# Performance work log

Hardware: AMD Instinct MI355X
Metric: run time of the kernel (lower is better)

The kernel has to match this reference:

```python
import jax, jax.numpy as jnp
import numpy as np

N, IN_F, OUT_F = 4096, 512, 16
HID = [128, 64, 32]
H = 4  # num_head
LRELU_SLOPE = 0.2
BN_EPS = 1e-5
NEG_INF = -1e9


def _gat(x, adj_mask, W, a_src, a_dst, heads, f_out):
    n = x.shape[0]
    h = (x @ W).reshape(n, heads, f_out)              # [N,H,F]
    es = jnp.einsum('nhf,hf->hn', h, a_src)           # [H,N]
    ed = jnp.einsum('nhf,hf->hn', h, a_dst)           # [H,N]
    e = jax.nn.leaky_relu(es[:, :, None] + ed[:, None, :], LRELU_SLOPE)  # [H,N,N]
    e = jnp.where(adj_mask[None], e, NEG_INF)
    attn = jax.nn.softmax(e, axis=-1)                 # masked softmax over neighbors
    out = jnp.einsum('hij,jhf->ihf', attn, h)         # [N,H,F]
    return out.reshape(n, heads * f_out)


def _bn_elu(x, gamma, beta):
    mu = jnp.mean(x, axis=0)
    var = jnp.var(x, axis=0)
    xhat = (x - mu) * jax.lax.rsqrt(var + BN_EPS)
    return jax.nn.elu(xhat * gamma + beta)


def setup_inputs() -> dict:
    key = jax.random.key(0)
    ks = jax.random.split(key, 14)
    s = lambda fin: 1.0 / np.sqrt(fin)
    x = jax.random.normal(ks[0], (N, IN_F), jnp.float32)
    adj = jax.random.randint(ks[1], (N, N), 0, 2, jnp.int32)
    W1 = jax.random.normal(ks[2], (IN_F, H * HID[0]), jnp.float32) * s(IN_F)
    a1s = jax.random.normal(ks[3], (H, HID[0]), jnp.float32) * s(HID[0])
    a1d = jax.random.normal(ks[4], (H, HID[0]), jnp.float32) * s(HID[0])
    lw1 = jax.random.normal(ks[5], (H * HID[0], HID[1]), jnp.float32) * s(H * HID[0])
    lb1 = jnp.zeros((HID[1],), jnp.float32)
    g1 = jnp.ones((HID[1],), jnp.float32)
    be1 = jnp.zeros((HID[1],), jnp.float32)
    W2 = jax.random.normal(ks[6], (HID[1], H * HID[2]), jnp.float32) * s(HID[1])
    a2s = jax.random.normal(ks[7], (H, HID[2]), jnp.float32) * s(HID[2])
    a2d = jax.random.normal(ks[8], (H, HID[2]), jnp.float32) * s(HID[2])
    lw2 = jax.random.normal(ks[9], (H * HID[2], OUT_F), jnp.float32) * s(H * HID[2])
    lb2 = jnp.zeros((OUT_F,), jnp.float32)
    g2 = jnp.ones((OUT_F,), jnp.float32)
    be2 = jnp.zeros((OUT_F,), jnp.float32)
    return dict(x=x, adj=adj, W1=W1, a1s=a1s, a1d=a1d, lw1=lw1, lb1=lb1, g1=g1, be1=be1,
                W2=W2, a2s=a2s, a2d=a2d, lw2=lw2, lb2=lb2, g2=g2, be2=be2)


def reference(x, adj, W1, a1s, a1d, lw1, lb1, g1, be1, W2, a2s, a2d, lw2, lb2, g2, be2):
    adj_mask = adj > 0
    x1 = _gat(x, adj_mask, W1, a1s, a1d, H, HID[0])        # [N, H*128]
    x2 = _bn_elu(x1 @ lw1 + lb1, g1, be1)                  # [N, 64]
    x3 = _gat(x2, adj_mask, W2, a2s, a2d, H, HID[2])       # [N, H*32]
    out = _bn_elu(x3 @ lw2 + lb2, g2, be2)                 # [N, 16]
    return out
```

## Files before the change

### kernel.cpp

```cpp
#include <hip/hip_runtime.h>
#include <hip/hip_bf16.h>
#include <stdint.h>

#define NN 4096
#define H4 4

typedef __hip_bfloat16 bf16;
typedef unsigned short ushort_t;
typedef unsigned long long ull_t;
typedef __attribute__((ext_vector_type(4))) float f32x4;
typedef __attribute__((ext_vector_type(8))) short s16x8;

__device__ __forceinline__ float cvt(float v) { return v; }
__device__ __forceinline__ float cvt(bf16 v) { return __bfloat162float(v); }
__device__ __forceinline__ ushort_t f2bf(float f) {
  unsigned u = __float_as_uint(f);
  return (ushort_t)((u + 0x7fff + ((u >> 16) & 1)) >> 16);
}
__device__ __forceinline__ float bf2f(ushort_t h) {
  return __uint_as_float((unsigned)h << 16);
}
__device__ __forceinline__ short2 pkbf(float a, float b) {
  union { __hip_bfloat162 h; short2 s; } u;
  u.h = __float22bfloat162_rn(make_float2(a, b));
  return u.s;
}
__device__ __forceinline__ s16x8 as_s16x8(uint4 v) {
  union { uint4 u; s16x8 s; } c; c.u = v; return c.s;
}

__global__ __launch_bounds__(256) void k_mask(const int* __restrict__ adj,
                                              ull_t* __restrict__ mask) {
  int row = blockIdx.x, tid = threadIdx.x;
  int lane = tid & 63, wv = tid >> 6;
  const int* arow = adj + (size_t)row * NN;
  for (int c = 0; c < NN; c += 256) {
    int col = c + wv * 64 + lane;
    ull_t b = __ballot(arow[col] != 0);
    if (lane == 0) mask[row * 64 + (c >> 6) + wv] = b;
  }
}

__global__ __launch_bounds__(256) void k_gemm(const float* __restrict__ A,
                                              const float* __restrict__ B,
                                              const float* __restrict__ bias,
                                              float* __restrict__ C, int M, int K, int Nc) {
  __shared__ float As[16][68];
  __shared__ float Bs[16][68];
  int tid = threadIdx.x;
  int tx = tid & 15, ty = tid >> 4;
  int mBase = blockIdx.y * 64, nBase = blockIdx.x * 64;
  float acc[4][4] = {};
  for (int k0 = 0; k0 < K; k0 += 16) {
#pragma unroll
    for (int l = 0; l < 4; ++l) {
      int idx = l * 256 + tid;
      int m = idx >> 4, k = idx & 15;
      As[k][m] = A[(size_t)(mBase + m) * K + (k0 + k)];
    }
#pragma unroll
    for (int l = 0; l < 4; ++l) {
      int idx = l * 256 + tid;
      int k = idx >> 6, n = idx & 63;
      int gn = nBase + n;
      Bs[k][n] = (gn < Nc) ? B[(size_t)(k0 + k) * Nc + gn] : 0.f;
    }
    __syncthreads();
#pragma unroll
    for (int k = 0; k < 16; ++k) {
      float4 a = *(const float4*)&As[k][ty * 4];
      float4 b = *(const float4*)&Bs[k][tx * 4];
      float av[4] = {a.x, a.y, a.z, a.w};
      float bv[4] = {b.x, b.y, b.z, b.w};
#pragma unroll
      for (int r = 0; r < 4; ++r)
#pragma unroll
        for (int c = 0; c < 4; ++c) acc[r][c] += av[r] * bv[c];
    }
    __syncthreads();
  }
#pragma unroll
  for (int r = 0; r < 4; ++r) {
    int gm = mBase + ty * 4 + r;
#pragma unroll
    for (int c = 0; c < 4; ++c) {
      int gn = nBase + tx * 4 + c;
      if (gn < Nc) {
        float v = acc[r][c];
        if (bias) v += bias[gn];
        C[(size_t)gm * Nc + gn] = v;
      }
    }
  }
}

#define APLANE (4096 * 512)
__global__ __launch_bounds__(256) void k_packA(const float* __restrict__ x,
                                               ushort_t* __restrict__ pkA) {
  int t = threadIdx.x;
  int w = t >> 6, lane = t & 63;
  int q = lane >> 4, nn = lane & 15;
  int tau = blockIdx.x * 4 + w;
  int mt = tau >> 4, ks = tau & 15;
  const float* src = &x[(size_t)(mt * 16 + nn) * 512 + ks * 32 + q * 8];
  float4 v0 = *(const float4*)src;
  float4 v1 = *(const float4*)(src + 4);
  float vv[8] = {v0.x, v0.y, v0.z, v0.w, v1.x, v1.y, v1.z, v1.w};
  ushort_t hi[8], lo[8];
#pragma unroll
  for (int u = 0; u < 8; ++u) {
    hi[u] = f2bf(vv[u]);
    lo[u] = f2bf(vv[u] - bf2f(hi[u]));
  }
  size_t idx = ((size_t)(mt * 16 + ks) * 64 + lane) * 8;
  *(uint4*)&pkA[idx] = *(uint4*)hi;
  *(uint4*)&pkA[APLANE + idx] = *(uint4*)lo;
}

template <int KK, int NC>
__global__ __launch_bounds__(256) void k_packWg(const float* __restrict__ W,
                                                ushort_t* __restrict__ pk) {
  constexpr int KS = KK / 32;
  constexpr int T = (NC / 16) * KS;
  constexpr int PL = T * 512;
  int t = threadIdx.x;
  int w = t >> 6, lane = t & 63;
  int q = lane >> 4, nn = lane & 15;
  int tau = blockIdx.x * 4 + w;
  if (tau >= T) return;
  int ct = tau / KS, ks = tau % KS;
  ushort_t hi[8], lo[8];
#pragma unroll
  for (int u = 0; u < 8; ++u) {
    float v = W[(size_t)(ks * 32 + q * 8 + u) * NC + ct * 16 + nn];
    hi[u] = f2bf(v);
    lo[u] = f2bf(v - bf2f(hi[u]));
  }
  size_t idx = ((size_t)(ct * KS + ks) * 64 + lane) * 8;
  *(uint4*)&pk[idx] = *(uint4*)hi;
  *(uint4*)&pk[PL + idx] = *(uint4*)lo;
}

__global__ __launch_bounds__(256, 1) void k_mm1(const uint4* __restrict__ pkA,
                                                const uint4* __restrict__ pkW,
                                                float* __restrict__ h1) {
  constexpr int APL4 = APLANE / 8;
  constexpr int WPL4 = (512 / 16) * (512 / 32) * 64;
  int t = threadIdx.x;
  int w = t >> 6, lane = t & 63;
  int q = lane >> 4, nn = lane & 15;
  int mt0 = blockIdx.x * 4 + (w & 1) * 2;
  int ct0 = blockIdx.y * 8 + (w >> 1) * 4;
  f32x4 acc[2][4];
#pragma unroll
  for (int rt = 0; rt < 2; ++rt)
#pragma unroll
    for (int c = 0; c < 4; ++c)
#pragma unroll
      for (int k = 0; k < 4; ++k) acc[rt][c][k] = 0.f;
#pragma unroll
  for (int ks = 0; ks < 16; ++ks) {
    int ia0 = (mt0 * 16 + ks) * 64 + lane;
    int ia1 = ((mt0 + 1) * 16 + ks) * 64 + lane;
    uint4 ah0 = pkA[ia0], ah1 = pkA[ia1];
    uint4 al0 = pkA[APL4 + ia0], al1 = pkA[APL4 + ia1];
    uint4 bh[4], bl[4];
#pragma unroll
    for (int c = 0; c < 4; ++c) {
      int ib = ((ct0 + c) * 16 + ks) * 64 + lane;
      bh[c] = pkW[ib];
      bl[c] = pkW[WPL4 + ib];
    }
#pragma unroll
    for (int c = 0; c < 4; ++c) {
      acc[0][c] = __builtin_amdgcn_mfma_f32_16x16x32_bf16(as_s16x8(ah0), as_s16x8(bh[c]), acc[0][c], 0, 0, 0);
      acc[0][c] = __builtin_amdgcn_mfma_f32_16x16x32_bf16(as_s16x8(ah0), as_s16x8(bl[c]), acc[0][c], 0, 0, 0);
      acc[0][c] = __builtin_amdgcn_mfma_f32_16x16x32_bf16(as_s16x8(al0), as_s16x8(bh[c]), acc[0][c], 0, 0, 0);
      acc[1][c] = __builtin_amdgcn_mfma_f32_16x16x32_bf16(as_s16x8(ah1), as_s16x8(bh[c]), acc[1][c], 0, 0, 0);
      acc[1][c] = __builtin_amdgcn_mfma_f32_16x16x32_bf16(as_s16x8(ah1), as_s16x8(bl[c]), acc[1][c], 0, 0, 0);
      acc[1][c] = __builtin_amdgcn_mfma_f32_16x16x32_bf16(as_s16x8(al1), as_s16x8(bh[c]), acc[1][c], 0, 0, 0);
    }
  }
  int rowB = blockIdx.x * 64 + (w & 1) * 32;
#pragma unroll
  for (int rt = 0; rt < 2; ++rt)
#pragma unroll
    for (int c = 0; c < 4; ++c)
#pragma unroll
      for (int reg = 0; reg < 4; ++reg) {
        int gi = rowB + rt * 16 + q * 4 + reg;
        h1[(size_t)gi * 512 + (ct0 + c) * 16 + nn] = acc[rt][c][reg];
      }
}

template <int F, int TB>
__global__ __launch_bounds__(TB) void k_pack(const float* __restrict__ h,
                                             ushort_t* __restrict__ pk) {
  constexpr int CTW = TB / 64;
  int t = threadIdx.x;
  int lane = t & 63, ctw = t >> 6;
  int q = lane >> 4, nn = lane & 15;
  int ks = blockIdx.x, hd = blockIdx.y;
#pragma unroll
  for (int ct = ctw; ct < F / 16; ct += CTW) {
    ushort_t v[8];
#pragma unroll
    for (int u = 0; u < 8; ++u)
      v[u] = f2bf(h[(size_t)(ks * 32 + q * 8 + u) * (H4 * F) + hd * F + ct * 16 + nn]);
    *(uint4*)&pk[((((size_t)hd * (F / 16) + ct) * (NN / 32) + ks) * 64 + lane) * 8] =
        *(uint4*)v;
  }
}

template <int F>
__global__ __launch_bounds__(256) void k_scores(const float* __restrict__ h,
                                                const float* __restrict__ a_s,
                                                const float* __restrict__ a_d,
                                                float* __restrict__ es, float* __restrict__ ed) {
  int idx = blockIdx.x * 256 + threadIdx.x;
  if (idx >= NN * H4) return;
  int n = idx >> 2, hd = idx & 3;
  const float* hp = h + (size_t)n * (H4 * F) + hd * F;
  const float* sp = a_s + hd * F;
  const float* dp = a_d + hd * F;
  float ss = 0.f, sd = 0.f;
#pragma unroll 4
  for (int f = 0; f < F; ++f) {
    float v = hp[f];
    ss += v * sp[f];
    sd += v * dp[f];
  }
  es[hd * NN + n] = ss;
  ed[hd * NN + n] = sd;
}

__device__ __forceinline__ s16x8 build_a(float esi, unsigned byt, float4 ea, float4 eb,
                                         float& rs) {
  float ev[8] = {ea.x, ea.y, ea.z, ea.w, eb.x, eb.y, eb.z, eb.w};
  union { s16x8 v; short2 p[4]; } A;
#pragma unroll
  for (int tp = 0; tp < 4; ++tp) {
    float z0 = esi + ev[2 * tp];
    z0 = fmaxf(z0, 0.2f * z0);
    float w0 = (byt & (1u << (2 * tp))) ? __expf(fminf(z0, 80.f)) : 0.f;
    float z1 = esi + ev[2 * tp + 1];
    z1 = fmaxf(z1, 0.2f * z1);
    float w1 = (byt & (1u << (2 * tp + 1))) ? __expf(fminf(z1, 80.f)) : 0.f;
    rs += w0 + w1;
    A.p[tp] = pkbf(w0, w1);
  }
  return A.v;
}

template <int F, int OUTM>
__global__ __launch_bounds__(256, 2) void k_agg_mfma(
    const uint4* __restrict__ pk, const float* __restrict__ es,
    const float* __restrict__ ed, const ull_t* __restrict__ mask,
    ushort_t* __restrict__ pkOut) {
  constexpr int CT = F / 16;
  constexpr int KSO = (H4 * F) / 32;
  constexpr int OPL = NN * H4 * F;
  __shared__ float red[2 * 32 * F];
  __shared__ float rsred[32 * 4];
  int t = threadIdx.x;
  int w = t >> 6, lane = t & 63;
  int q = lane >> 4, nn = lane & 15;
  int hd = blockIdx.y;
  int rowBase = blockIdx.x * 32;
  int jBase = w * (NN / 4);
  int ia0 = rowBase + nn, ia1 = rowBase + 16 + nn;
  float es0 = es[hd * NN + ia0];
  float es1 = es[hd * NN + ia1];
  const ull_t* mk0p = mask + (size_t)ia0 * 64;
  const ull_t* mk1p = mask + (size_t)ia1 * 64;
  const float* edh = ed + hd * NN;

  f32x4 acc[2][CT];
#pragma unroll
  for (int rt = 0; rt < 2; ++rt)
#pragma unroll
    for (int cc = 0; cc < CT; ++cc)
#pragma unroll
      for (int k = 0; k < 4; ++k) acc[rt][cc][k] = 0.f;
  float rs0 = 0.f, rs1 = 0.f;

  for (int jc = 0; jc < NN / 4 / 64; ++jc) {
    int j0 = jBase + jc * 64;
    int ks0 = j0 >> 5;
    uint4 bv[2][CT];
#pragma unroll
    for (int s = 0; s < 2; ++s)
#pragma unroll
      for (int cc = 0; cc < CT; ++cc)
        bv[s][cc] = pk[(size_t)((hd * CT + cc) * (NN / 32) + ks0 + s) * 64 + lane];
    ull_t mk0 = mk0p[j0 >> 6], mk1 = mk1p[j0 >> 6];
    float4 e0 = *(const float4*)&edh[j0 + q * 8];
    float4 e1 = *(const float4*)&edh[j0 + q * 8 + 4];
    float4 e2 = *(const float4*)&edh[j0 + 32 + q * 8];
    float4 e3 = *(const float4*)&edh[j0 + 32 + q * 8 + 4];
    s16x8 a00 = build_a(es0, (unsigned)(mk0 >> (q * 8)) & 0xffu, e0, e1, rs0);
    s16x8 a01 = build_a(es0, (unsigned)(mk0 >> (32 + q * 8)) & 0xffu, e2, e3, rs0);
    s16x8 a10 = build_a(es1, (unsigned)(mk1 >> (q * 8)) & 0xffu, e0, e1, rs1);
    s16x8 a11 = build_a(es1, (unsigned)(mk1 >> (32 + q * 8)) & 0xffu, e2, e3, rs1);
#pragma unroll
    for (int cc = 0; cc < CT; ++cc)
      acc[0][cc] = __builtin_amdgcn_mfma_f32_16x16x32_bf16(a00, as_s16x8(bv[0][cc]), acc[0][cc], 0, 0, 0);
#pragma unroll
    for (int cc = 0; cc < CT; ++cc)
      acc[0][cc] = __builtin_amdgcn_mfma_f32_16x16x32_bf16(a01, as_s16x8(bv[1][cc]), acc[0][cc], 0, 0, 0);
#pragma unroll
    for (int cc = 0; cc < CT; ++cc)
      acc[1][cc] = __builtin_amdgcn_mfma_f32_16x16x32_bf16(a10, as_s16x8(bv[0][cc]), acc[1][cc], 0, 0, 0);
#pragma unroll
    for (int cc = 0; cc < CT; ++cc)
      acc[1][cc] = __builtin_amdgcn_mfma_f32_16x16x32_bf16(a11, as_s16x8(bv[1][cc]), acc[1][cc], 0, 0, 0);
  }

  rs0 += __shfl_xor(rs0, 16, 64); rs0 += __shfl_xor(rs0, 32, 64);
  rs1 += __shfl_xor(rs1, 16, 64); rs1 += __shfl_xor(rs1, 32, 64);
  if (q == 0) {
    rsred[nn * 4 + w] = rs0;
    rsred[(16 + nn) * 4 + w] = rs1;
  }

#define IDX(rt, cc, reg) ((rt * 16 + q * 4 + reg) * F + cc * 16 + nn)
  if (w == 1 || w == 3) {
    int base = (w >> 1) * 32 * F;
#pragma unroll
    for (int rt = 0; rt < 2; ++rt)
#pragma unroll
      for (int cc = 0; cc < CT; ++cc)
#pragma unroll
        for (int reg = 0; reg < 4; ++reg) red[base + IDX(rt, cc, reg)] = acc[rt][cc][reg];
  }
  __syncthreads();
  if (w == 0 || w == 2) {
    int base = (w >> 1) * 32 * F;
#pragma unroll
    for (int rt = 0; rt < 2; ++rt)
#pragma unroll
      for (int cc = 0; cc < CT; ++cc)
#pragma unroll
        for (int reg = 0; reg < 4; ++reg) acc[rt][cc][reg] += red[base + IDX(rt, cc, reg)];
  }
  if (w == 2) {
#pragma unroll
    for (int rt = 0; rt < 2; ++rt)
#pragma unroll
      for (int cc = 0; cc < CT; ++cc)
#pragma unroll
        for (int reg = 0; reg < 4; ++reg) red[32 * F + IDX(rt, cc, reg)] = acc[rt][cc][reg];
  }
  __syncthreads();
  if (w == 0) {
    float rinv[2][4];
#pragma unroll
    for (int rt = 0; rt < 2; ++rt)
#pragma unroll
      for (int reg = 0; reg < 4; ++reg) {
        int row = rt * 16 + q * 4 + reg;
        float4 rv = *(float4*)&rsred[row * 4];
        float s = (rv.x + rv.y) + (rv.z + rv.w);
        rinv[rt][reg] = (s > 0.f) ? 1.f / s : 0.f;
      }
#pragma unroll
    for (int rt = 0; rt < 2; ++rt)
#pragma unroll
      for (int cc = 0; cc < CT; ++cc)
#pragma unroll
        for (int reg = 0; reg < 4; ++reg) {
          float v = (acc[rt][cc][reg] + red[32 * F + IDX(rt, cc, reg)]) * rinv[rt][reg];
          int gi = rowBase + rt * 16 + q * 4 + reg;
          int c = hd * F + cc * 16 + nn;
          int mt = gi >> 4, rowin = gi & 15;
          int ks = c >> 5, qp = (c >> 3) & 3, u = c & 7;
          size_t idx = (((size_t)mt * KSO + ks) * 64 + qp * 16 + rowin) * 8 + u;
          ushort_t hi = f2bf(v);
          pkOut[idx] = hi;
          if (OUTM == 1) pkOut[OPL + idx] = f2bf(v - bf2f(hi));
        }
  }
#undef IDX
}

__global__ __launch_bounds__(256) void k_mm2(const uint4* __restrict__ pkX,
                                             const uint4* __restrict__ pkW,
                                             const float* __restrict__ bias,
                                             float* __restrict__ y) {
  constexpr int WPL4 = 4 * 16 * 64;
  __shared__ float red[2 * 16 * 64];
  int t = threadIdx.x;
  int w = t >> 6, lane = t & 63;
  int q = lane >> 4, nn = lane & 15;
  int mt = blockIdx.x * 2 + (w & 1);
  int kh = w >> 1;
  f32x4 acc[4];
#pragma unroll
  for (int c = 0; c < 4; ++c)
#pragma unroll
    for (int k = 0; k < 4; ++k) acc[c][k] = 0.f;
#pragma unroll
  for (int k8 = 0; k8 < 8; ++k8) {
    int ks = kh * 8 + k8;
    uint4 a = pkX[(mt * 16 + ks) * 64 + lane];
#pragma unroll
    for (int c = 0; c < 4; ++c) {
      uint4 bh = pkW[(c * 16 + ks) * 64 + lane];
      uint4 bl = pkW[WPL4 + (c * 16 + ks) * 64 + lane];
      acc[c] = __builtin_amdgcn_mfma_f32_16x16x32_bf16(as_s16x8(a), as_s16x8(bh), acc[c], 0, 0, 0);
      acc[c] = __builtin_amdgcn_mfma_f32_16x16x32_bf16(as_s16x8(a), as_s16x8(bl), acc[c], 0, 0, 0);
    }
  }
  int base = (w & 1) * 1024;
  if (kh == 1) {
#pragma unroll
    for (int c = 0; c < 4; ++c)
#pragma unroll
      for (int reg = 0; reg < 4; ++reg)
        red[base + (q * 4 + reg) * 64 + c * 16 + nn] = acc[c][reg];
  }
  __syncthreads();
  if (kh == 0) {
#pragma unroll
    for (int c = 0; c < 4; ++c)
#pragma unroll
      for (int reg = 0; reg < 4; ++reg) {
        float v = acc[c][reg] + red[base + (q * 4 + reg) * 64 + c * 16 + nn] + bias[c * 16 + nn];
        y[(size_t)(mt * 16 + q * 4 + reg) * 64 + c * 16 + nn] = v;
      }
  }
}

__global__ __launch_bounds__(256) void k_mm4(const uint4* __restrict__ pkX,
                                             const uint4* __restrict__ pkW,
                                             const float* __restrict__ bias,
                                             float* __restrict__ y) {
  constexpr int XPL4 = 256 * 4 * 64;
  constexpr int WPL4 = 1 * 4 * 64;
  int t = threadIdx.x;
  int w = t >> 6, lane = t & 63;
  int q = lane >> 4, nn = lane & 15;
  int mt = blockIdx.x * 4 + w;
  f32x4 acc;
#pragma unroll
  for (int k = 0; k < 4; ++k) acc[k] = 0.f;
#pragma unroll
  for (int ks = 0; ks < 4; ++ks) {
    uint4 ah = pkX[(mt * 4 + ks) * 64 + lane];
    uint4 al = pkX[XPL4 + (mt * 4 + ks) * 64 + lane];
    uint4 bh = pkW[ks * 64 + lane];
    uint4 bl = pkW[WPL4 + ks * 64 + lane];
    acc = __builtin_amdgcn_mfma_f32_16x16x32_bf16(as_s16x8(ah), as_s16x8(bh), acc, 0, 0, 0);
    acc = __builtin_amdgcn_mfma_f32_16x16x32_bf16(as_s16x8(ah), as_s16x8(bl), acc, 0, 0, 0);
    acc = __builtin_amdgcn_mfma_f32_16x16x32_bf16(as_s16x8(al), as_s16x8(bh), acc, 0, 0, 0);
  }
  float b = bias[nn];
#pragma unroll
  for (int reg = 0; reg < 4; ++reg)
    y[(size_t)(mt * 16 + q * 4 + reg) * 16 + nn] = acc[reg] + b;
}

__global__ __launch_bounds__(256) void k_colstats(const float* __restrict__ y,
                                                  float* __restrict__ stats, int C) {
  int c = blockIdx.x, tid = threadIdx.x;
  float s = 0.f, s2 = 0.f;
  for (int r = tid; r < NN; r += 256) {
    float v = y[(size_t)r * C + c];
    s += v;
    s2 += v * v;
  }
  __shared__ float sh[256], sh2[256];
  sh[tid] = s; sh2[tid] = s2;
  __syncthreads();
  for (int off = 128; off; off >>= 1) {
    if (tid < off) { sh[tid] += sh[tid + off]; sh2[tid] += sh2[tid + off]; }
    __syncthreads();
  }
  if (tid == 0) {
    float mean = sh[0] * (1.f / NN);
    float var = sh2[0] * (1.f / NN) - mean * mean;
    stats[c] = mean;
    stats[C + c] = rsqrtf(fmaxf(var, 0.f) + 1e-5f);
  }
}

__global__ __launch_bounds__(256) void k_bn_elu(const float* __restrict__ y,
                                                const float* __restrict__ stats,
                                                const float* __restrict__ gamma,
                                                const float* __restrict__ beta,
                                                float* __restrict__ o, int C, int total) {
  int idx = blockIdx.x * 256 + threadIdx.x;
  if (idx >= total) return;
  int c = idx % C;
  float v = (y[idx] - stats[c]) * stats[C + c] * gamma[c] + beta[c];
  v = v > 0.f ? v : (__expf(v) - 1.f);
  o[idx] = v;
}

extern "C" void kernel_launch(void* const* d_in, const int* in_sizes, int n_in,
                              void* d_out, int out_size, void* d_ws, size_t ws_size,
                              hipStream_t stream) {
  (void)in_sizes; (void)n_in; (void)out_size; (void)ws_size;
  const float* x   = (const float*)d_in[0];
  const int*   adj = (const int*)d_in[1];
  const float* W1  = (const float*)d_in[2];
  const float* a1s = (const float*)d_in[3];
  const float* a1d = (const float*)d_in[4];
  const float* lw1 = (const float*)d_in[5];
  const float* lb1 = (const float*)d_in[6];
  const float* g1  = (const float*)d_in[7];
  const float* be1 = (const float*)d_in[8];
  const float* W2  = (const float*)d_in[9];
  const float* a2s = (const float*)d_in[10];
  const float* a2d = (const float*)d_in[11];
  const float* lw2 = (const float*)d_in[12];
  const float* lb2 = (const float*)d_in[13];
  const float* g2  = (const float*)d_in[14];
  const float* be2 = (const float*)d_in[15];
  float* out = (float*)d_out;

  char* w = (char*)d_ws;
  const size_t MB = 1u << 20;
  ull_t*    mask  = (ull_t*)(w + 0);
  ushort_t* pkA   = (ushort_t*)(w + 2 * MB);
  ushort_t* pkW1  = (ushort_t*)(w + 10 * MB);
  float*    h1    = (float*)(w + 11 * MB);
  ushort_t* pk1   = (ushort_t*)(w + 19 * MB);
  float*    es1   = (float*)(w + 23 * MB);
  float*    ed1   = (float*)(w + 23 * MB + 65536);
  ushort_t* pkX1  = (ushort_t*)(w + 24 * MB);
  ushort_t* pkLW1 = (ushort_t*)(w + 28 * MB);
  float*    y1    = (float*)(w + 29 * MB);
  float*    x2    = (float*)(w + 30 * MB);
  float*    h2    = (float*)(w + 31 * MB);
  ushort_t* pk2   = (ushort_t*)(w + 33 * MB);
  float*    es2   = (float*)(w + 34 * MB);
  float*    ed2   = (float*)(w + 34 * MB + 65536);
  ushort_t* pkX3  = (ushort_t*)(w + 35 * MB);
  ushort_t* pkLW2 = (ushort_t*)(w + 37 * MB);
  float*    y2    = (float*)(w + 37 * MB + 131072);
  float*    st1   = (float*)(w + 38 * MB);
  float*    st2   = (float*)(w + 38 * MB + 4096);

  k_mask<<<NN, 256, 0, stream>>>(adj, mask);

  k_packA<<<1024, 256, 0, stream>>>(x, pkA);
  k_packWg<512, 512><<<128, 256, 0, stream>>>(W1, pkW1);
  k_packWg<512, 64><<<16, 256, 0, stream>>>(lw1, pkLW1);
  k_packWg<128, 16><<<1, 256, 0, stream>>>(lw2, pkLW2);
  k_mm1<<<dim3(64, 4), 256, 0, stream>>>((const uint4*)pkA, (const uint4*)pkW1, h1);
  k_pack<128, 256><<<dim3(NN / 32, H4), 256, 0, stream>>>(h1, pk1);
  k_scores<128><<<(NN * H4) / 256, 256, 0, stream>>>(h1, a1s, a1d, es1, ed1);
  k_agg_mfma<128, 0><<<dim3(128, H4), 256, 0, stream>>>((const uint4*)pk1, es1, ed1, mask,
                                                        pkX1);

  k_mm2<<<128, 256, 0, stream>>>((const uint4*)pkX1, (const uint4*)pkLW1, lb1, y1);
  k_colstats<<<64, 256, 0, stream>>>(y1, st1, 64);
  k_bn_elu<<<(NN * 64) / 256, 256, 0, stream>>>(y1, st1, g1, be1, x2, 64, NN * 64);

  k_gemm<<<dim3(2, 64), 256, 0, stream>>>(x2, W2, nullptr, h2, NN, 64, 128);
  k_pack<32, 128><<<dim3(NN / 32, H4), 128, 0, stream>>>(h2, pk2);
  k_scores<32><<<(NN * H4) / 256, 256, 0, stream>>>(h2, a2s, a2d, es2, ed2);
  k_agg_mfma<32, 1><<<dim3(128, H4), 256, 0, stream>>>((const uint4*)pk2, es2, ed2, mask,
                                                       pkX3);

  k_mm4<<<64, 256, 0, stream>>>((const uint4*)pkX3, (const uint4*)pkLW2, lb2, y2);
  k_colstats<<<16, 256, 0, stream>>>(y2, st2, 16);
  k_bn_elu<<<(NN * 16) / 256, 256, 0, stream>>>(y2, st2, g2, be2, out, 16, NN * 16);
}
```

Measured before the change: 297.1 us.

## Factor attention exp into per-node terms, halve agg tile, merge pack and BN kernels

Attention weights are rewritten as exp(leakyrelu(s+d)) = exp(s)*exp(d) or exp(.2s)*exp(.2d), selected by comparing exp(d) with exp(-s). The exponentials are precomputed per node in the score kernel, so the aggregation inner loop needs no transcendentals. The aggregation kernel now handles 16 rows per block instead of 32, with twice as many blocks and a higher occupancy bound. The four input-packing kernels are merged into one launch, and the column-stats and BN-ELU kernels are fused into a single per-column kernel. Scores are clamped to ±30, which can change results for large logits, and the per-column BN kernel reads memory with a column stride.

```diff
diff --git a/kernel.cpp b/kernel.cpp
--- a/kernel.cpp
+++ b/kernel.cpp
@@ -11,8 +11,6 @@
 typedef __attribute__((ext_vector_type(4))) float f32x4;
 typedef __attribute__((ext_vector_type(8))) short s16x8;
 
-__device__ __forceinline__ float cvt(float v) { return v; }
-__device__ __forceinline__ float cvt(bf16 v) { return __bfloat162float(v); }
 __device__ __forceinline__ ushort_t f2bf(float f) {
   unsigned u = __float_as_uint(f);
   return (ushort_t)((u + 0x7fff + ((u >> 16) & 1)) >> 16);
@@ -95,39 +93,14 @@
 }
 
 #define APLANE (4096 * 512)
-__global__ __launch_bounds__(256) void k_packA(const float* __restrict__ x,
-                                               ushort_t* __restrict__ pkA) {
-  int t = threadIdx.x;
-  int w = t >> 6, lane = t & 63;
-  int q = lane >> 4, nn = lane & 15;
-  int tau = blockIdx.x * 4 + w;
-  int mt = tau >> 4, ks = tau & 15;
-  const float* src = &x[(size_t)(mt * 16 + nn) * 512 + ks * 32 + q * 8];
-  float4 v0 = *(const float4*)src;
-  float4 v1 = *(const float4*)(src + 4);
-  float vv[8] = {v0.x, v0.y, v0.z, v0.w, v1.x, v1.y, v1.z, v1.w};
-  ushort_t hi[8], lo[8];
-#pragma unroll
-  for (int u = 0; u < 8; ++u) {
-    hi[u] = f2bf(vv[u]);
-    lo[u] = f2bf(vv[u] - bf2f(hi[u]));
-  }
-  size_t idx = ((size_t)(mt * 16 + ks) * 64 + lane) * 8;
-  *(uint4*)&pkA[idx] = *(uint4*)hi;
-  *(uint4*)&pkA[APLANE + idx] = *(uint4*)lo;
-}
-
 template <int KK, int NC>
-__global__ __launch_bounds__(256) void k_packWg(const float* __restrict__ W,
-                                                ushort_t* __restrict__ pk) {
+__device__ __forceinline__ void packW_dev(const float* __restrict__ W,
+                                          ushort_t* __restrict__ pk, int tau, int lane) {
   constexpr int KS = KK / 32;
   constexpr int T = (NC / 16) * KS;
   constexpr int PL = T * 512;
-  int t = threadIdx.x;
-  int w = t >> 6, lane = t & 63;
+  if (tau >= T) return;
   int q = lane >> 4, nn = lane & 15;
-  int tau = blockIdx.x * 4 + w;
-  if (tau >= T) return;
   int ct = tau / KS, ks = tau % KS;
   ushort_t hi[8], lo[8];
 #pragma unroll
@@ -139,6 +112,42 @@
   size_t idx = ((size_t)(ct * KS + ks) * 64 + lane) * 8;
   *(uint4*)&pk[idx] = *(uint4*)hi;
   *(uint4*)&pk[PL + idx] = *(uint4*)lo;
+}
+
+__global__ __launch_bounds__(256) void k_packP(const float* __restrict__ x,
+                                               const float* __restrict__ W1,
+                                               const float* __restrict__ lw1,
+                                               const float* __restrict__ lw2,
+                                               ushort_t* __restrict__ pkA,
+                                               ushort_t* __restrict__ pkW1,
+                                               ushort_t* __restrict__ pkLW1,
+                                               ushort_t* __restrict__ pkLW2) {
+  int b = blockIdx.x, t = threadIdx.x;
+  int w = t >> 6, lane = t & 63;
+  if (b < 1024) {
+    int q = lane >> 4, nn = lane & 15;
+    int tau = b * 4 + w;
+    int mt = tau >> 4, ks = tau & 15;
+    const float* src = &x[(size_t)(mt * 16 + nn) * 512 + ks * 32 + q * 8];
+    float4 v0 = *(const float4*)src;
+    float4 v1 = *(const float4*)(src + 4);
+    float vv[8] = {v0.x, v0.y, v0.z, v0.w, v1.x, v1.y, v1.z, v1.w};
+    ushort_t hi[8], lo[8];
+#pragma unroll
+    for (int u = 0; u < 8; ++u) {
+      hi[u] = f2bf(vv[u]);
+      lo[u] = f2bf(vv[u] - bf2f(hi[u]));
+    }
+    size_t idx = ((size_t)(mt * 16 + ks) * 64 + lane) * 8;
+    *(uint4*)&pkA[idx] = *(uint4*)hi;
+    *(uint4*)&pkA[APLANE + idx] = *(uint4*)lo;
+  } else if (b < 1152) {
+    packW_dev<512, 512>(W1, pkW1, (b - 1024) * 4 + w, lane);
+  } else if (b < 1168) {
+    packW_dev<512, 64>(lw1, pkLW1, (b - 1152) * 4 + w, lane);
+  } else {
+    packW_dev<128, 16>(lw2, pkLW2, (b - 1168) * 4 + w, lane);
+  }
 }
 
 __global__ __launch_bounds__(256, 1) void k_mm1(const uint4* __restrict__ pkA,
@@ -216,7 +225,9 @@
 __global__ __launch_bounds__(256) void k_scores(const float* __restrict__ h,
                                                 const float* __restrict__ a_s,
                                                 const float* __restrict__ a_d,
-                                                float* __restrict__ es, float* __restrict__ ed) {
+                                                float* __restrict__ Tt, float* __restrict__ E1,
+                                                float* __restrict__ E2, float* __restrict__ D1,
+                                                float* __restrict__ D2) {
   int idx = blockIdx.x * 256 + threadIdx.x;
   if (idx >= NN * H4) return;
   int n = idx >> 2, hd = idx & 3;
@@ -230,155 +241,154 @@
     ss += v * sp[f];
     sd += v * dp[f];
   }
-  es[hd * NN + n] = ss;
-  ed[hd * NN + n] = sd;
-}
-
-__device__ __forceinline__ s16x8 build_a(float esi, unsigned byt, float4 ea, float4 eb,
-                                         float& rs) {
-  float ev[8] = {ea.x, ea.y, ea.z, ea.w, eb.x, eb.y, eb.z, eb.w};
+  ss = fminf(fmaxf(ss, -30.f), 30.f);
+  sd = fminf(fmaxf(sd, -30.f), 30.f);
+  int o = hd * NN + n;
+  Tt[o] = __expf(-ss);
+  E1[o] = __expf(ss);
+  E2[o] = __expf(0.2f * ss);
+  D1[o] = __expf(sd);
+  D2[o] = __expf(0.2f * sd);
+}
+
+__device__ __forceinline__ s16x8 build_af(float E1i, float E2i, float Ti, unsigned byt,
+                                          float4 d1a, float4 d1b, float4 d2a, float4 d2b,
+                                          float& rs) {
+  float d1[8] = {d1a.x, d1a.y, d1a.z, d1a.w, d1b.x, d1b.y, d1b.z, d1b.w};
+  float d2[8] = {d2a.x, d2a.y, d2a.z, d2a.w, d2b.x, d2b.y, d2b.z, d2b.w};
   union { s16x8 v; short2 p[4]; } A;
 #pragma unroll
   for (int tp = 0; tp < 4; ++tp) {
-    float z0 = esi + ev[2 * tp];
-    z0 = fmaxf(z0, 0.2f * z0);
-    float w0 = (byt & (1u << (2 * tp))) ? __expf(fminf(z0, 80.f)) : 0.f;
-    float z1 = esi + ev[2 * tp + 1];
-    z1 = fmaxf(z1, 0.2f * z1);
-    float w1 = (byt & (1u << (2 * tp + 1))) ? __expf(fminf(z1, 80.f)) : 0.f;
-    rs += w0 + w1;
-    A.p[tp] = pkbf(w0, w1);
+    int k0 = 2 * tp, k1 = 2 * tp + 1;
+    bool p0 = d1[k0] > Ti;
+    float u0 = (p0 ? E1i : E2i) * (p0 ? d1[k0] : d2[k0]);
+    u0 = (byt & (1u << k0)) ? u0 : 0.f;
+    bool p1 = d1[k1] > Ti;
+    float u1 = (p1 ? E1i : E2i) * (p1 ? d1[k1] : d2[k1]);
+    u1 = (byt & (1u << k1)) ? u1 : 0.f;
+    rs += u0 + u1;
+    A.p[tp] = pkbf(u0, u1);
   }
   return A.v;
 }
 
 template <int F, int OUTM>
-__global__ __launch_bounds__(256, 2) void k_agg_mfma(
-    const uint4* __restrict__ pk, const float* __restrict__ es,
-    const float* __restrict__ ed, const ull_t* __restrict__ mask,
-    ushort_t* __restrict__ pkOut) {
+__global__ __launch_bounds__(256, 4) void k_agg_mfma(
+    const uint4* __restrict__ pk, const float* __restrict__ Tt,
+    const float* __restrict__ E1, const float* __restrict__ E2,
+    const float* __restrict__ D1, const float* __restrict__ D2,
+    const ull_t* __restrict__ mask, ushort_t* __restrict__ pkOut) {
   constexpr int CT = F / 16;
   constexpr int KSO = (H4 * F) / 32;
   constexpr int OPL = NN * H4 * F;
-  __shared__ float red[2 * 32 * F];
-  __shared__ float rsred[32 * 4];
+  __shared__ float red[2 * 16 * F];
+  __shared__ float rsred[16 * 4];
   int t = threadIdx.x;
   int w = t >> 6, lane = t & 63;
   int q = lane >> 4, nn = lane & 15;
   int hd = blockIdx.y;
-  int rowBase = blockIdx.x * 32;
+  int rowBase = blockIdx.x * 16;
   int jBase = w * (NN / 4);
-  int ia0 = rowBase + nn, ia1 = rowBase + 16 + nn;
-  float es0 = es[hd * NN + ia0];
-  float es1 = es[hd * NN + ia1];
-  const ull_t* mk0p = mask + (size_t)ia0 * 64;
-  const ull_t* mk1p = mask + (size_t)ia1 * 64;
-  const float* edh = ed + hd * NN;
-
-  f32x4 acc[2][CT];
-#pragma unroll
-  for (int rt = 0; rt < 2; ++rt)
-#pragma unroll
-    for (int cc = 0; cc < CT; ++cc)
-#pragma unroll
-      for (int k = 0; k < 4; ++k) acc[rt][cc][k] = 0.f;
-  float rs0 = 0.f, rs1 = 0.f;
+  int ia = rowBase + nn;
+  float E1i = E1[hd * NN + ia];
+  float E2i = E2[hd * NN + ia];
+  float Ti = Tt[hd * NN + ia];
+  const ull_t* mkp = mask + (size_t)ia * 64;
+  const float* d1h = D1 + hd * NN;
+  const float* d2h = D2 + hd * NN;
+
+  f32x4 acc[CT];
+#pragma unroll
+  for (int cc = 0; cc < CT; ++cc)
+#pragma unroll
+    for (int k = 0; k < 4; ++k) acc[cc][k] = 0.f;
+  float rs = 0.f;
 
   for (int jc = 0; jc < NN / 4 / 64; ++jc) {
     int j0 = jBase + jc * 64;
     int ks0 = j0 >> 5;
-    uint4 bv[2][CT];
-#pragma unroll
-    for (int s = 0; s < 2; ++s)
-#pragma unroll
-      for (int cc = 0; cc < CT; ++cc)
-        bv[s][cc] = pk[(size_t)((hd * CT + cc) * (NN / 32) + ks0 + s) * 64 + lane];
-    ull_t mk0 = mk0p[j0 >> 6], mk1 = mk1p[j0 >> 6];
-    float4 e0 = *(const float4*)&edh[j0 + q * 8];
-    float4 e1 = *(const float4*)&edh[j0 + q * 8 + 4];
-    float4 e2 = *(const float4*)&edh[j0 + 32 + q * 8];
-    float4 e3 = *(const float4*)&edh[j0 + 32 + q * 8 + 4];
-    s16x8 a00 = build_a(es0, (unsigned)(mk0 >> (q * 8)) & 0xffu, e0, e1, rs0);
-    s16x8 a01 = build_a(es0, (unsigned)(mk0 >> (32 + q * 8)) & 0xffu, e2, e3, rs0);
-    s16x8 a10 = build_a(es1, (unsigned)(mk1 >> (q * 8)) & 0xffu, e0, e1, rs1);
-    s16x8 a11 = build_a(es1, (unsigned)(mk1 >> (32 + q * 8)) & 0xffu, e2, e3, rs1);
-#pragma unroll
-    for (int cc = 0; cc < CT; ++cc)
-      acc[0][cc] = __builtin_amdgcn_mfma_f32_16x16x32_bf16(a00, as_s16x8(bv[0][cc]), acc[0][cc], 0, 0, 0);
-#pragma unroll
-    for (int cc = 0; cc < CT; ++cc)
-      acc[0][cc] = __builtin_amdgcn_mfma_f32_16x16x32_bf16(a01, as_s16x8(bv[1][cc]), acc[0][cc], 0, 0, 0);
-#pragma unroll
-    for (int cc = 0; cc < CT; ++cc)
-      acc[1][cc] = __builtin_amdgcn_mfma_f32_16x16x32_bf16(a10, as_s16x8(bv[0][cc]), acc[1][cc], 0, 0, 0);
-#pragma unroll
-    for (int cc = 0; cc < CT; ++cc)
-      acc[1][cc] = __builtin_amdgcn_mfma_f32_16x16x32_bf16(a11, as_s16x8(bv[1][cc]), acc[1][cc], 0, 0, 0);
-  }
-
-  rs0 += __shfl_xor(rs0, 16, 64); rs0 += __shfl_xor(rs0, 32, 64);
-  rs1 += __shfl_xor(rs1, 16, 64); rs1 += __shfl_xor(rs1, 32, 64);
-  if (q == 0) {
-    rsred[nn * 4 + w] = rs0;
-    rsred[(16 + nn) * 4 + w] = rs1;
-  }
-
-#define IDX(rt, cc, reg) ((rt * 16 + q * 4 + reg) * F + cc * 16 + nn)
-  if (w == 1 || w == 3) {
-    int base = (w >> 1) * 32 * F;
-#pragma unroll
-    for (int rt = 0; rt < 2; ++rt)
-#pragma unroll
-      for (int cc = 0; cc < CT; ++cc)
-#pragma unroll
-        for (int reg = 0; reg < 4; ++reg) red[base + IDX(rt, cc, reg)] = acc[rt][cc][reg];
-  }
-  __syncthreads();
-  if (w == 0 || w == 2) {
-    int base = (w >> 1) * 32 * F;
-#pragma unroll
-    for (int rt = 0; rt < 2; ++rt)
-#pragma unroll
-      for (int cc = 0; cc < CT; ++cc)
-#pragma unroll
-        for (int reg = 0; reg < 4; ++reg) acc[rt][cc][reg] += red[base + IDX(rt, cc, reg)];
-  }
-  if (w == 2) {
-#pragma unroll
-    for (int rt = 0; rt < 2; ++rt)
-#pragma unroll
-      for (int cc = 0; cc < CT; ++cc)
-#pragma unroll
-        for (int reg = 0; reg < 4; ++reg) red[32 * F + IDX(rt, cc, reg)] = acc[rt][cc][reg];
+    ull_t mk = mkp[j0 >> 6];
+    float4 d1a = *(const float4*)&d1h[j0 + q * 8];
+    float4 d1b = *(const float4*)&d1h[j0 + q * 8 + 4];
+    float4 d2a = *(const float4*)&d2h[j0 + q * 8];
+    float4 d2b = *(const float4*)&d2h[j0 + q * 8 + 4];
+    float4 d1c = *(const float4*)&d1h[j0 + 32 + q * 8];
+    float4 d1d = *(const float4*)&d1h[j0 + 32 + q * 8 + 4];
+    float4 d2c = *(const float4*)&d2h[j0 + 32 + q * 8];
+    float4 d2d = *(const float4*)&d2h[j0 + 32 + q * 8 + 4];
+    s16x8 a0 = build_af(E1i, E2i, Ti, (unsigned)(mk >> (q * 8)) & 0xffu, d1a, d1b, d2a, d2b, rs);
+    s16x8 a1 = build_af(E1i, E2i, Ti, (unsigned)(mk >> (32 + q * 8)) & 0xffu, d1c, d1d, d2c, d2d, rs);
+    uint4 bv[CT];
+#pragma unroll
+    for (int cc = 0; cc < CT; ++cc)
+      bv[cc] = pk[(size_t)((hd * CT + cc) * (NN / 32) + ks0) * 64 + lane];
+#pragma unroll
+    for (int cc = 0; cc < CT; ++cc)
+      acc[cc] = __builtin_amdgcn_mfma_f32_16x16x32_bf16(a0, as_s16x8(bv[cc]), acc[cc], 0, 0, 0);
+#pragma unroll
+    for (int cc = 0; cc < CT; ++cc)
+      bv[cc] = pk[(size_t)((hd * CT + cc) * (NN / 32) + ks0 + 1) * 64 + lane];
+#pragma unroll
+    for (int cc = 0; cc < CT; ++cc)
+      acc[cc] = __builtin_amdgcn_mfma_f32_16x16x32_bf16(a1, as_s16x8(bv[cc]), acc[cc], 0, 0, 0);
+  }
+
+  rs += __shfl_xor(rs, 16, 64);
+  rs += __shfl_xor(rs, 32, 64);
+  if (q == 0) rsred[nn * 4 + w] = rs;
+
+#define IDX(cc, reg) (((q * 4 + reg) * F) + cc * 16 + nn)
+  if (w == 1) {
+#pragma unroll
+    for (int cc = 0; cc < CT; ++cc)
+#pragma unroll
+      for (int reg = 0; reg < 4; ++reg) red[IDX(cc, reg)] = acc[cc][reg];
+  }
+  if (w == 3) {
+#pragma unroll
+    for (int cc = 0; cc < CT; ++cc)
+#pragma unroll
+      for (int reg = 0; reg < 4; ++reg) red[16 * F + IDX(cc, reg)] = acc[cc][reg];
   }
   __syncthreads();
   if (w == 0) {
-    float rinv[2][4];
-#pragma unroll
-    for (int rt = 0; rt < 2; ++rt)
+#pragma unroll
+    for (int cc = 0; cc < CT; ++cc)
+#pragma unroll
+      for (int reg = 0; reg < 4; ++reg) acc[cc][reg] += red[IDX(cc, reg)];
+  }
+  if (w == 2) {
+#pragma unroll
+    for (int cc = 0; cc < CT; ++cc)
 #pragma unroll
       for (int reg = 0; reg < 4; ++reg) {
-        int row = rt * 16 + q * 4 + reg;
-        float4 rv = *(float4*)&rsred[row * 4];
-        float s = (rv.x + rv.y) + (rv.z + rv.w);
-        rinv[rt][reg] = (s > 0.f) ? 1.f / s : 0.f;
+        acc[cc][reg] += red[16 * F + IDX(cc, reg)];
+        red[16 * F + IDX(cc, reg)] = acc[cc][reg];
       }
-#pragma unroll
-    for (int rt = 0; rt < 2; ++rt)
-#pragma unroll
-      for (int cc = 0; cc < CT; ++cc)
-#pragma unroll
-        for (int reg = 0; reg < 4; ++reg) {
-          float v = (acc[rt][cc][reg] + red[32 * F + IDX(rt, cc, reg)]) * rinv[rt][reg];
-          int gi = rowBase + rt * 16 + q * 4 + reg;
-          int c = hd * F + cc * 16 + nn;
-          int mt = gi >> 4, rowin = gi & 15;
-          int ks = c >> 5, qp = (c >> 3) & 3, u = c & 7;
-          size_t idx = (((size_t)mt * KSO + ks) * 64 + qp * 16 + rowin) * 8 + u;
-          ushort_t hi = f2bf(v);
-          pkOut[idx] = hi;
-          if (OUTM == 1) pkOut[OPL + idx] = f2bf(v - bf2f(hi));
-        }
+  }
+  __syncthreads();
+  if (w == 0) {
+    float rinv[4];
+#pragma unroll
+    for (int reg = 0; reg < 4; ++reg) {
+      float4 rv = *(float4*)&rsred[(q * 4 + reg) * 4];
+      float s = (rv.x + rv.y) + (rv.z + rv.w);
+      rinv[reg] = (s > 0.f) ? 1.f / s : 0.f;
+    }
+#pragma unroll
+    for (int cc = 0; cc < CT; ++cc)
+#pragma unroll
+      for (int reg = 0; reg < 4; ++reg) {
+        float v = (acc[cc][reg] + red[16 * F + IDX(cc, reg)]) * rinv[reg];
+        int gi = rowBase + q * 4 + reg;
+        int c = hd * F + cc * 16 + nn;
+        int mt = gi >> 4, rowin = gi & 15;
+        int ks = c >> 5, qp = (c >> 3) & 3, u = c & 7;
+        size_t idx = (((size_t)mt * KSO + ks) * 64 + qp * 16 + rowin) * 8 + u;
+        ushort_t hi = f2bf(v);
+        pkOut[idx] = hi;
+        if (OUTM == 1) pkOut[OPL + idx] = f2bf(v - bf2f(hi));
+      }
   }
 #undef IDX
 }
@@ -460,8 +470,10 @@
     y[(size_t)(mt * 16 + q * 4 + reg) * 16 + nn] = acc[reg] + b;
 }
 
-__global__ __launch_bounds__(256) void k_colstats(const float* __restrict__ y,
-                                                  float* __restrict__ stats, int C) {
+__global__ __launch_bounds__(256) void k_bn_col(const float* __restrict__ y,
+                                                const float* __restrict__ gamma,
+                                                const float* __restrict__ beta,
+                                                float* __restrict__ o, int C) {
   int c = blockIdx.x, tid = threadIdx.x;
   float s = 0.f, s2 = 0.f;
   for (int r = tid; r < NN; r += 256) {
@@ -470,6 +482,7 @@
     s2 += v * v;
   }
   __shared__ float sh[256], sh2[256];
+  __shared__ float smu, srs;
   sh[tid] = s; sh2[tid] = s2;
   __syncthreads();
   for (int off = 128; off; off >>= 1) {
@@ -477,24 +490,18 @@
     __syncthreads();
   }
   if (tid == 0) {
-    float mean = sh[0] * (1.f / NN);
-    float var = sh2[0] * (1.f / NN) - mean * mean;
-    stats[c] = mean;
-    stats[C + c] = rsqrtf(fmaxf(var, 0.f) + 1e-5f);
-  }
-}
-
-__global__ __launch_bounds__(256) void k_bn_elu(const float* __restrict__ y,
-                                                const float* __restrict__ stats,
-                                                const float* __restrict__ gamma,
-                                                const float* __restrict__ beta,
-                                                float* __restrict__ o, int C, int total) {
-  int idx = blockIdx.x * 256 + threadIdx.x;
-  if (idx >= total) return;
-  int c = idx % C;
-  float v = (y[idx] - stats[c]) * stats[C + c] * gamma[c] + beta[c];
-  v = v > 0.f ? v : (__expf(v) - 1.f);
-  o[idx] = v;
+    float mu = sh[0] * (1.f / NN);
+    float var = sh2[0] * (1.f / NN) - mu * mu;
+    smu = mu;
+    srs = rsqrtf(fmaxf(var, 0.f) + 1e-5f);
+  }
+  __syncthreads();
+  float mu = smu, rstd = srs, g = gamma[c], b = beta[c];
+  for (int r = tid; r < NN; r += 256) {
+    float v = (y[(size_t)r * C + c] - mu) * rstd * g + b;
+    v = v > 0.f ? v : (__expf(v) - 1.f);
+    o[(size_t)r * C + c] = v;
+  }
 }
 
 extern "C" void kernel_launch(void* const* d_in, const int* in_sizes, int n_in,
@@ -526,45 +533,44 @@
   ushort_t* pkW1  = (ushort_t*)(w + 10 * MB);
   float*    h1    = (float*)(w + 11 * MB);
   ushort_t* pk1   = (ushort_t*)(w + 19 * MB);
-  float*    es1   = (float*)(w + 23 * MB);
-  float*    ed1   = (float*)(w + 23 * MB + 65536);
+  float*    T1    = (float*)(w + 23 * MB);
+  float*    E1a   = T1 + 16384;
+  float*    E2a   = E1a + 16384;
+  float*    D1a   = E2a + 16384;
+  float*    D2a   = D1a + 16384;
   ushort_t* pkX1  = (ushort_t*)(w + 24 * MB);
   ushort_t* pkLW1 = (ushort_t*)(w + 28 * MB);
   float*    y1    = (float*)(w + 29 * MB);
   float*    x2    = (float*)(w + 30 * MB);
   float*    h2    = (float*)(w + 31 * MB);
   ushort_t* pk2   = (ushort_t*)(w + 33 * MB);
-  float*    es2   = (float*)(w + 34 * MB);
-  float*    ed2   = (float*)(w + 34 * MB + 65536);
+  float*    T2    = (float*)(w + 34 * MB);
+  float*    E1b   = T2 + 16384;
+  float*    E2b   = E1b + 16384;
+  float*    D1b   = E2b + 16384;
+  float*    D2b   = D1b + 16384;
   ushort_t* pkX3  = (ushort_t*)(w + 35 * MB);
   ushort_t* pkLW2 = (ushort_t*)(w + 37 * MB);
   float*    y2    = (float*)(w + 37 * MB + 131072);
-  float*    st1   = (float*)(w + 38 * MB);
-  float*    st2   = (float*)(w + 38 * MB + 4096);
 
   k_mask<<<NN, 256, 0, stream>>>(adj, mask);
-
-  k_packA<<<1024, 256, 0, stream>>>(x, pkA);
-  k_packWg<512, 512><<<128, 256, 0, stream>>>(W1, pkW1);
-  k_packWg<512, 64><<<16, 256, 0, stream>>>(lw1, pkLW1);
-  k_packWg<128, 16><<<1, 256, 0, stream>>>(lw2, pkLW2);
+  k_packP<<<1169, 256, 0, stream>>>(x, W1, lw1, lw2, pkA, pkW1, pkLW1, pkLW2);
+
   k_mm1<<<dim3(64, 4), 256, 0, stream>>>((const uint4*)pkA, (const uint4*)pkW1, h1);
   k_pack<128, 256><<<dim3(NN / 32, H4), 256, 0, stream>>>(h1, pk1);
-  k_scores<128><<<(NN * H4) / 256, 256, 0, stream>>>(h1, a1s, a1d, es1, ed1);
-  k_agg_mfma<128, 0><<<dim3(128, H4), 256, 0, stream>>>((const uint4*)pk1, es1, ed1, mask,
-                                                        pkX1);
+  k_scores<128><<<(NN * H4) / 256, 256, 0, stream>>>(h1, a1s, a1d, T1, E1a, E2a, D1a, D2a);
+  k_agg_mfma<128, 0><<<dim3(NN / 16, H4), 256, 0, stream>>>((const uint4*)pk1, T1, E1a, E2a,
+                                                            D1a, D2a, mask, pkX1);
 
   k_mm2<<<128, 256, 0, stream>>>((const uint4*)pkX1, (const uint4*)pkLW1, lb1, y1);
-  k_colstats<<<64, 256, 0, stream>>>(y1, st1, 64);
-  k_bn_elu<<<(NN * 64) / 256, 256, 0, stream>>>(y1, st1, g1, be1, x2, 64, NN * 64);
+  k_bn_col<<<64, 256, 0, stream>>>(y1, g1, be1, x2, 64);
 
   k_gemm<<<dim3(2, 64), 256, 0, stream>>>(x2, W2, nullptr, h2, NN, 64, 128);
   k_pack<32, 128><<<dim3(NN / 32, H4), 128, 0, stream>>>(h2, pk2);
-  k_scores<32><<<(NN * H4) / 256, 256, 0, stream>>>(h2, a2s, a2d, es2, ed2);
-  k_agg_mfma<32, 1><<<dim3(128, H4), 256, 0, stream>>>((const uint4*)pk2, es2, ed2, mask,
-                                                       pkX3);
+  k_scores<32><<<(NN * H4) / 256, 256, 0, stream>>>(h2, a2s, a2d, T2, E1b, E2b, D1b, D2b);
+  k_agg_mfma<32, 1><<<dim3(NN / 16, H4), 256, 0, stream>>>((const uint4*)pk2, T2, E1b, E2b,
+                                                           D1b, D2b, mask, pkX3);
 
   k_mm4<<<64, 256, 0, stream>>>((const uint4*)pkX3, (const uint4*)pkLW2, lb2, y2);
-  k_colstats<<<16, 256, 0, stream>>>(y2, st2, 16);
-  k_bn_elu<<<(NN * 16) / 256, 256, 0, stream>>>(y2, st2, g2, be2, out, 16, NN * 16);
-}
+  k_bn_col<<<16, 256, 0, stream>>>(y2, g2, be2, out, 16);
+}
```

Result: slower. 329.4 us (+10.9%).
